# Kernel optimization log

Hardware: AMD Instinct MI355X
Metric: run time of the kernel (lower is better)

## Reference

```python
import jax, jax.numpy as jnp
import numpy as np

EPS_MSG = 1e-7   # GENConv message eps
EPS_LN = 1e-5    # LayerNorm eps

N, F_IN, D, D_OUT = 32768, 64, 512, 128


def setup_inputs() -> dict:
    key = jax.random.key(0)
    ks = jax.random.split(key, 20)
    s = 0.02
    inp = {
        "batch": jax.random.normal(ks[0], (1, N, F_IN), jnp.float32),
        "W_enc": jax.random.normal(ks[1], (F_IN, D), jnp.float32) * s,
        "b_enc": jnp.zeros((D,), jnp.float32),
        "Wf": jax.random.normal(ks[2], (D, D_OUT), jnp.float32) * s,
        "bf": jnp.zeros((D_OUT,), jnp.float32),
    }
    for l in range(2):
        inp[f"t{l}"] = jnp.array(1.0, jnp.float32)           # learnable softmax temperature
        inp[f"W1_{l}"] = jax.random.normal(ks[3 + 6 * l], (D, 2 * D), jnp.float32) * s
        inp[f"b1_{l}"] = jnp.zeros((2 * D,), jnp.float32)
        inp[f"g_{l}"] = jnp.ones((2 * D,), jnp.float32)      # LN gamma
        inp[f"be_{l}"] = jnp.zeros((2 * D,), jnp.float32)    # LN beta
        inp[f"W2_{l}"] = jax.random.normal(ks[4 + 6 * l], (2 * D, D), jnp.float32) * s
        inp[f"b2_{l}"] = jnp.zeros((D,), jnp.float32)
    return inp


def _layer_norm(z, g, b):
    mu = jnp.mean(z, axis=-1, keepdims=True)
    var = jnp.var(z, axis=-1, keepdims=True)
    return (z - mu) * jax.lax.rsqrt(var + EPS_LN) * g + b


def _deepgcn_layer(x, t, W1, b1, g, be, W2, b2):
    # res+ block: h = conv(act(norm(x))); return x + h   (norm is Identity here)
    h = jax.nn.relu(x)                       # [n, d]
    # GENConv with complete graph: msg_j = relu(h_j) + eps (independent of target i)
    m = jax.nn.relu(h) + EPS_MSG             # [n, d]
    alpha = jax.nn.softmax(t * m, axis=0)    # per-channel softmax over all source nodes
    agg = jnp.sum(alpha * m, axis=0)         # [d]  -- identical for every target node
    out = h + agg[None, :]                   # + x_dst residual inside GENConv
    # GENConv MLP: Linear(d,2d) -> LayerNorm -> ReLU -> Linear(2d,d)
    z = jax.nn.relu(_layer_norm(out @ W1 + b1, g, be))
    out = z @ W2 + b2
    return x + out


def reference(batch, W_enc, b_enc, Wf, bf,
              t0, W1_0, b1_0, g_0, be_0, W2_0, b2_0,
              t1, W1_1, b1_1, g_1, be_1, W2_1, b2_1):
    bsz, n, _ = batch.shape
    x = batch.reshape(bsz * n, -1) @ W_enc + b_enc   # node encoder
    x = _deepgcn_layer(x, t0, W1_0, b1_0, g_0, be_0, W2_0, b2_0)
    x = _deepgcn_layer(x, t1, W1_1, b1_1, g_1, be_1, W2_1, b2_1)
    x = jax.nn.relu(x)                               # layers[0].act(layers[0].norm(x)), norm=Identity
    out = x @ Wf + bf
    return out.reshape(bsz, n, -1)
```

## Files before the change

kernel.cpp:

```cpp
#include <hip/hip_runtime.h>

#define DEV __device__ __forceinline__

typedef __attribute__((ext_vector_type(8))) short s8v;
typedef __attribute__((ext_vector_type(4))) float f4v;

DEV short f2bf(float f) {
  unsigned u = __builtin_bit_cast(unsigned, f);
  u += 0x7fffu + ((u >> 16) & 1u);
  return (short)(u >> 16);
}
DEV float bf2f(short s) {
  unsigned u = ((unsigned)(unsigned short)s) << 16;
  return __builtin_bit_cast(float, u);
}

DEV f4v mfma_16x16x32_bf16(s8v a, s8v b, f4v c) {
  asm("v_mfma_f32_16x16x32_bf16 %0, %1, %2, %0" : "+v"(c) : "v"(a), "v"(b));
  return c;
}

DEV s8v relu8(s8v a) {
#pragma unroll
  for (int i = 0; i < 8; ++i) a[i] = a[i] > (short)0 ? a[i] : (short)0;
  return a;
}

__global__ __launch_bounds__(256) void tconv_k(const float* __restrict__ in,
                                               short* __restrict__ out,
                                               int K, int N) {
  __shared__ float t[64][65];
  const int nb = blockIdx.x * 64, kb = blockIdx.y * 64;
  const int c = threadIdx.x & 63, r0 = threadIdx.x >> 6;
#pragma unroll
  for (int rr = 0; rr < 64; rr += 4)
    t[rr + r0][c] = in[(size_t)(kb + rr + r0) * N + nb + c];
  __syncthreads();
#pragma unroll
  for (int rr = 0; rr < 64; rr += 4)
    out[(size_t)(nb + rr + r0) * K + kb + c] = f2bf(t[c][rr + r0]);
}

__global__ __launch_bounds__(256) void conv_k(const float* __restrict__ in,
                                              short* __restrict__ out, int n4) {
  int i = blockIdx.x * 256 + threadIdx.x;
  if (i >= n4) return;
  float4 v = ((const float4*)in)[i];
  short4 o;
  o.x = f2bf(v.x);
  o.y = f2bf(v.y);
  o.z = f2bf(v.z);
  o.w = f2bf(v.w);
  ((short4*)out)[i] = o;
}

__global__ __launch_bounds__(256) void zero_k(float* p, int n) {
  int i = blockIdx.x * 256 + threadIdx.x;
  if (i < n) p[i] = 0.f;
}

__global__ __launch_bounds__(256) void finalize_k(const float* __restrict__ sums,
                                                  const float* __restrict__ W1,
                                                  const float* __restrict__ b1,
                                                  float* __restrict__ biasEff) {
  __shared__ float agg[512];
  __shared__ float part[16][16];
  const int tid = threadIdx.x;
  for (int d = tid; d < 512; d += 256) agg[d] = sums[512 + d] / sums[d];
  __syncthreads();
  const int j = blockIdx.x * 16 + (tid & 15);
  const int grp = tid >> 4;
  float p = 0.f;
#pragma unroll 4
  for (int dd = 0; dd < 32; ++dd) {
    int d = grp * 32 + dd;
    p += agg[d] * W1[(size_t)d * 1024 + j];
  }
  part[grp][tid & 15] = p;
  __syncthreads();
  if (tid < 16) {
    float a = b1[blockIdx.x * 16 + tid];
#pragma unroll
    for (int g = 0; g < 16; ++g) a += part[g][tid];
    biasEff[blockIdx.x * 16 + tid] = a;
  }
}

__global__ __launch_bounds__(256) void ln_relu_k(short* __restrict__ z,
                                                 const float* __restrict__ g,
                                                 const float* __restrict__ be) {
  const int row = blockIdx.x * 4 + (threadIdx.x >> 6);
  const int lane = threadIdx.x & 63;
  short* zr = z + (size_t)row * 1024;
  s8v c0 = *(const s8v*)&zr[lane * 8];
  s8v c1 = *(const s8v*)&zr[512 + lane * 8];
  float v[16];
  float s = 0.f, q = 0.f;
#pragma unroll
  for (int i = 0; i < 8; ++i) { v[i] = bf2f(c0[i]); v[8 + i] = bf2f(c1[i]); }
#pragma unroll
  for (int i = 0; i < 16; ++i) { s += v[i]; q += v[i] * v[i]; }
#pragma unroll
  for (int o = 32; o > 0; o >>= 1) { s += __shfl_xor(s, o); q += __shfl_xor(q, o); }
  float mu = s * (1.f / 1024.f);
  float var = q * (1.f / 1024.f) - mu * mu;
  float rs = rsqrtf(var + 1e-5f);
  float gv[16], bv[16];
#pragma unroll
  for (int i = 0; i < 8; ++i) {
    gv[i] = g[lane * 8 + i];      gv[8 + i] = g[512 + lane * 8 + i];
    bv[i] = be[lane * 8 + i];     bv[8 + i] = be[512 + lane * 8 + i];
  }
  s8v o0, o1;
#pragma unroll
  for (int i = 0; i < 8; ++i) {
    o0[i] = f2bf(fmaxf((v[i] - mu) * rs * gv[i] + bv[i], 0.f));
    o1[i] = f2bf(fmaxf((v[8 + i] - mu) * rs * gv[8 + i] + bv[8 + i], 0.f));
  }
  *(s8v*)&zr[lane * 8] = o0;
  *(s8v*)&zr[512 + lane * 8] = o1;
}

#define F_ADD   1
#define F_WF32  2
#define F_WBF   4
#define F_SM    8
#define F_RELUA 16

template <int FLAGS>
__global__ __launch_bounds__(256) void gemm_k(const short* __restrict__ A,
                                              const short* __restrict__ Bt,
                                              const float* __restrict__ bias,
                                              const short* __restrict__ Xin,
                                              short* __restrict__ Cb,
                                              float* __restrict__ Cf,
                                              const float* __restrict__ tptr,
                                              float* __restrict__ sums,
                                              int M, int N, int K) {
  __shared__ short lA[128 * 64];
  __shared__ short lB[128 * 64];
  const int tid = threadIdx.x;
  const int lane = tid & 63, wid = tid >> 6;
  const int wr = wid >> 1, wc = wid & 1;
  const int nwg = gridDim.x * gridDim.y;
  const int wg = blockIdx.y * gridDim.x + blockIdx.x;
  const int swz = (wg & 7) * (nwg >> 3) + (wg >> 3);
  const int bx = swz % gridDim.x, by = swz / gridDim.x;
  const int brow = by * 128, bcol = bx * 128;
  const int l15 = lane & 15, lhi = lane >> 4;
  f4v acc[4][4] = {};

  for (int k0 = 0; k0 < K; k0 += 64) {
#pragma unroll
    for (int r = 0; r < 4; ++r) {
      int chunk = r * 256 + tid;
      int row = chunk >> 3;
      int kc = ((chunk & 7) ^ (row & 7)) << 3;
      const short* ga = A + (size_t)(brow + row) * K + (k0 + kc);
      const short* gb = Bt + (size_t)(bcol + row) * K + (k0 + kc);
      __builtin_amdgcn_global_load_lds(
          (const __attribute__((address_space(1))) void*)ga,
          (__attribute__((address_space(3))) void*)&lA[(r * 256 + wid * 64) * 8],
          16, 0, 0);
      __builtin_amdgcn_global_load_lds(
          (const __attribute__((address_space(1))) void*)gb,
          (__attribute__((address_space(3))) void*)&lB[(r * 256 + wid * 64) * 8],
          16, 0, 0);
    }
    __syncthreads();
#pragma unroll
    for (int kk = 0; kk < 2; ++kk) {
      s8v af[4], bfr[4];
#pragma unroll
      for (int i = 0; i < 4; ++i) {
        const int rowA = wr * 64 + i * 16 + l15;
        const int rowB = wc * 64 + i * 16 + l15;
        const int cA = ((kk * 4 + lhi) ^ (rowA & 7)) << 3;
        const int cB = ((kk * 4 + lhi) ^ (rowB & 7)) << 3;
        af[i]  = *(const s8v*)&lA[rowA * 64 + cA];
        bfr[i] = *(const s8v*)&lB[rowB * 64 + cB];
        if (FLAGS & F_RELUA) af[i] = relu8(af[i]);
      }
#pragma unroll
      for (int mi = 0; mi < 4; ++mi)
#pragma unroll
        for (int ni = 0; ni < 4; ++ni)
          acc[mi][ni] = mfma_16x16x32_bf16(af[mi], bfr[ni], acc[mi][ni]);
    }
    __syncthreads();
  }

  const float tv = (FLAGS & F_SM) ? tptr[0] : 0.f;
  float* sred = (float*)lA;
  if (FLAGS & F_SM) {
    sred[tid] = 0.f;
    __syncthreads();
  }
#pragma unroll
  for (int ni = 0; ni < 4; ++ni) {
    int col = bcol + wc * 64 + ni * 16 + l15;
    float bv = bias[col];
    float se = 0.f, sem = 0.f;
#pragma unroll
    for (int mi = 0; mi < 4; ++mi) {
#pragma unroll
      for (int r = 0; r < 4; ++r) {
        int row = brow + wr * 64 + mi * 16 + lhi * 4 + r;
        size_t idx = (size_t)row * N + col;
        float v = acc[mi][ni][r] + bv;
        if (FLAGS & F_ADD) v += bf2f(Xin[idx]);
        if (FLAGS & F_WF32) Cf[idx] = v;
        if (FLAGS & F_WBF) Cb[idx] = f2bf(v);
        if (FLAGS & F_SM) {
          float m = fmaxf(v, 0.f) + 1e-7f;
          float e = __expf(tv * m);
          se += e;
          sem += e * m;
        }
      }
    }
    if (FLAGS & F_SM) {
      se += __shfl_xor(se, 16);   se += __shfl_xor(se, 32);
      sem += __shfl_xor(sem, 16); sem += __shfl_xor(sem, 32);
      if (lhi == 0) {
        atomicAdd(&sred[wc * 64 + ni * 16 + l15], se);
        atomicAdd(&sred[128 + wc * 64 + ni * 16 + l15], sem);
      }
    }
  }
  if (FLAGS & F_SM) {
    __syncthreads();
    int v = tid >> 7, c = tid & 127;
    atomicAdd(&sums[v * 512 + bcol + c], sred[v * 128 + c]);
  }
}

extern "C" void kernel_launch(void* const* d_in, const int* in_sizes, int n_in,
                              void* d_out, int out_size, void* d_ws,
                              size_t ws_size, hipStream_t stream) {
  (void)in_sizes; (void)n_in; (void)out_size; (void)ws_size;
  const float* batch = (const float*)d_in[0];
  const float* W_enc = (const float*)d_in[1];
  const float* b_enc = (const float*)d_in[2];
  const float* Wf    = (const float*)d_in[3];
  const float* bfv   = (const float*)d_in[4];
  const float* tptr[2] = {(const float*)d_in[5],  (const float*)d_in[12]};
  const float* W1[2]   = {(const float*)d_in[6],  (const float*)d_in[13]};
  const float* b1[2]   = {(const float*)d_in[7],  (const float*)d_in[14]};
  const float* g[2]    = {(const float*)d_in[8],  (const float*)d_in[15]};
  const float* be[2]   = {(const float*)d_in[9],  (const float*)d_in[16]};
  const float* W2[2]   = {(const float*)d_in[10], (const float*)d_in[17]};
  const float* b2[2]   = {(const float*)d_in[11], (const float*)d_in[18]};
  float* out = (float*)d_out;

  const int M = 32768;
  char* ws = (char*)d_ws;
  size_t off = 0;
  auto alloc = [&](size_t bytes) -> char* {
    char* p = ws + off;
    off += (bytes + 255) & ~(size_t)255;
    return p;
  };
  short* xbf    = (short*)alloc((size_t)M * 512 * 2);
  short* zbuf   = (short*)alloc((size_t)M * 1024 * 2);
  short* bbuf   = (short*)alloc((size_t)M * 64 * 2);
  short* wencT  = (short*)alloc(512 * 64 * 2);
  short* w1T0   = (short*)alloc(1024 * 512 * 2);
  short* w2T0   = (short*)alloc(512 * 1024 * 2);
  short* w1T1   = (short*)alloc(1024 * 512 * 2);
  short* w2T1   = (short*)alloc(512 * 1024 * 2);
  short* wfT    = (short*)alloc(128 * 512 * 2);
  float* sums   = (float*)alloc(2 * 1024 * 4);
  float* biasEff= (float*)alloc(1024 * 4);
  short* w1T[2] = {w1T0, w1T1};
  short* w2T[2] = {w2T0, w2T1};

  tconv_k<<<dim3(512 / 64, 64 / 64), 256, 0, stream>>>(W_enc, wencT, 64, 512);
  tconv_k<<<dim3(1024 / 64, 512 / 64), 256, 0, stream>>>(W1[0], w1T[0], 512, 1024);
  tconv_k<<<dim3(512 / 64, 1024 / 64), 256, 0, stream>>>(W2[0], w2T[0], 1024, 512);
  tconv_k<<<dim3(1024 / 64, 512 / 64), 256, 0, stream>>>(W1[1], w1T[1], 512, 1024);
  tconv_k<<<dim3(512 / 64, 1024 / 64), 256, 0, stream>>>(W2[1], w2T[1], 1024, 512);
  tconv_k<<<dim3(128 / 64, 512 / 64), 256, 0, stream>>>(Wf, wfT, 512, 128);

  conv_k<<<(M * 64 / 4 + 255) / 256, 256, 0, stream>>>(batch, bbuf, M * 64 / 4);
  zero_k<<<(2048 + 255) / 256, 256, 0, stream>>>(sums, 2048);

  gemm_k<F_WBF | F_SM><<<dim3(512 / 128, M / 128), 256, 0, stream>>>(
      bbuf, wencT, b_enc, nullptr, xbf, nullptr, tptr[0], sums, M, 512, 64);

  for (int l = 0; l < 2; ++l) {
    finalize_k<<<64, 256, 0, stream>>>(sums + l * 1024, W1[l], b1[l], biasEff);
    gemm_k<F_WBF | F_RELUA><<<dim3(1024 / 128, M / 128), 256, 0, stream>>>(
        xbf, w1T[l], biasEff, nullptr, zbuf, nullptr, nullptr, nullptr,
        M, 1024, 512);
    ln_relu_k<<<M / 4, 256, 0, stream>>>(zbuf, g[l], be[l]);
    if (l == 0) {
      gemm_k<F_ADD | F_WBF | F_SM><<<dim3(512 / 128, M / 128), 256, 0, stream>>>(
          zbuf, w2T[l], b2[l], xbf, xbf, nullptr, tptr[1], sums + 1024,
          M, 512, 1024);
    } else {
      gemm_k<F_ADD | F_WBF><<<dim3(512 / 128, M / 128), 256, 0, stream>>>(
          zbuf, w2T[l], b2[l], xbf, xbf, nullptr, nullptr, nullptr,
          M, 512, 1024);
    }
  }

  gemm_k<F_WF32 | F_RELUA><<<dim3(128 / 128, M / 128), 256, 0, stream>>>(
      xbf, wfT, bfv, nullptr, nullptr, out, nullptr, nullptr, M, 128, 512);
}
```

Baseline: 371.6 us.

## Double-buffer LDS tiles in GEMM with explicit vmcnt waits and barriers

Splits the GEMM main loop into stage/compute phases over two LDS buffer pairs. The next K-tile's global-to-LDS loads are issued while the current tile is consumed, with explicit s_waitcnt vmcnt and s_barrier instead of __syncthreads. It also raises wave priority during the MFMA phase. This aims to hide global load latency behind matrix math, at the cost of doubling LDS use to 64KB per block, which may reduce occupancy.

```diff
diff --git a/kernel.cpp b/kernel.cpp
--- a/kernel.cpp
+++ b/kernel.cpp
@@ -127,6 +127,11 @@
 #define F_SM    8
 #define F_RELUA 16
 
+#define VM8  asm volatile("s_waitcnt vmcnt(8)" ::: "memory")
+#define VM0  asm volatile("s_waitcnt vmcnt(0)" ::: "memory")
+#define SBAR __builtin_amdgcn_s_barrier()
+#define SCH0 __builtin_amdgcn_sched_barrier(0)
+
 template <int FLAGS>
 __global__ __launch_bounds__(256) void gemm_k(const short* __restrict__ A,
                                               const short* __restrict__ Bt,
@@ -137,8 +142,10 @@
                                               const float* __restrict__ tptr,
                                               float* __restrict__ sums,
                                               int M, int N, int K) {
-  __shared__ short lA[128 * 64];
-  __shared__ short lB[128 * 64];
+  __shared__ short lA0[128 * 64];
+  __shared__ short lB0[128 * 64];
+  __shared__ short lA1[128 * 64];
+  __shared__ short lB1[128 * 64];
   const int tid = threadIdx.x;
   const int lane = tid & 63, wid = tid >> 6;
   const int wr = wid >> 1, wc = wid & 1;
@@ -150,7 +157,8 @@
   const int l15 = lane & 15, lhi = lane >> 4;
   f4v acc[4][4] = {};
 
-  for (int k0 = 0; k0 < K; k0 += 64) {
+  auto stage = [&](short* dA, short* dB, int t) {
+    const int k0 = t << 6;
 #pragma unroll
     for (int r = 0; r < 4; ++r) {
       int chunk = r * 256 + tid;
@@ -160,14 +168,17 @@
       const short* gb = Bt + (size_t)(bcol + row) * K + (k0 + kc);
       __builtin_amdgcn_global_load_lds(
           (const __attribute__((address_space(1))) void*)ga,
-          (__attribute__((address_space(3))) void*)&lA[(r * 256 + wid * 64) * 8],
+          (__attribute__((address_space(3))) void*)&dA[(r * 256 + wid * 64) * 8],
           16, 0, 0);
       __builtin_amdgcn_global_load_lds(
           (const __attribute__((address_space(1))) void*)gb,
-          (__attribute__((address_space(3))) void*)&lB[(r * 256 + wid * 64) * 8],
+          (__attribute__((address_space(3))) void*)&dB[(r * 256 + wid * 64) * 8],
           16, 0, 0);
     }
-    __syncthreads();
+  };
+
+  auto compute = [&](const short* lA, const short* lB) {
+    __builtin_amdgcn_s_setprio(1);
 #pragma unroll
     for (int kk = 0; kk < 2; ++kk) {
       s8v af[4], bfr[4];
@@ -187,11 +198,29 @@
         for (int ni = 0; ni < 4; ++ni)
           acc[mi][ni] = mfma_16x16x32_bf16(af[mi], bfr[ni], acc[mi][ni]);
     }
-    __syncthreads();
+    __builtin_amdgcn_s_setprio(0);
+  };
+
+  const int nt = K >> 6;
+  stage(lA0, lB0, 0);
+  if (nt > 1) { stage(lA1, lB1, 1); VM8; } else { VM0; }
+  SCH0; SBAR;
+
+  for (int t = 0; t < nt; t += 2) {
+    compute(lA0, lB0);
+    SBAR;
+    if (t + 2 < nt) { stage(lA0, lB0, t + 2); VM8; } else { VM0; }
+    SCH0; SBAR;
+    if (t + 1 < nt) {
+      compute(lA1, lB1);
+      SBAR;
+      if (t + 3 < nt) { stage(lA1, lB1, t + 3); VM8; } else { VM0; }
+      SCH0; SBAR;
+    }
   }
 
   const float tv = (FLAGS & F_SM) ? tptr[0] : 0.f;
-  float* sred = (float*)lA;
+  float* sred = (float*)lA0;
   if (FLAGS & F_SM) {
     sred[tid] = 0.f;
     __syncthreads();
```

New measurement: 376.9 us. Within noise of the previous version (+1.4%).

## Fuse first MLP GEMM with LayerNorm and ReLU epilogue

Applied to the files above, without the earlier changes.

Replaces the W1 GEMM plus separate LayerNorm/ReLU kernel with a single kernel where each 1024-thread block computes full 1024-wide rows for 64 nodes, then reduces row statistics across waves in shared memory and applies LN, gamma/beta and ReLU before writing bf16. This removes one full read-modify-write pass over the large intermediate z buffer and a kernel launch per layer. In exchange, the new GEMM uses a small K-step with no double buffering, reloads the whole weight slab per block, and launches fewer, larger blocks, which may lower MFMA efficiency.

```diff
diff --git a/kernel.cpp b/kernel.cpp
--- a/kernel.cpp
+++ b/kernel.cpp
@@ -25,6 +25,12 @@
   for (int i = 0; i < 8; ++i) a[i] = a[i] > (short)0 ? a[i] : (short)0;
   return a;
 }
+
+#define F_ADD   1
+#define F_WF32  2
+#define F_WBF   4
+#define F_SM    8
+#define F_RELUA 16
 
 __global__ __launch_bounds__(256) void tconv_k(const float* __restrict__ in,
                                                short* __restrict__ out,
@@ -85,47 +91,6 @@
     biasEff[blockIdx.x * 16 + tid] = a;
   }
 }
-
-__global__ __launch_bounds__(256) void ln_relu_k(short* __restrict__ z,
-                                                 const float* __restrict__ g,
-                                                 const float* __restrict__ be) {
-  const int row = blockIdx.x * 4 + (threadIdx.x >> 6);
-  const int lane = threadIdx.x & 63;
-  short* zr = z + (size_t)row * 1024;
-  s8v c0 = *(const s8v*)&zr[lane * 8];
-  s8v c1 = *(const s8v*)&zr[512 + lane * 8];
-  float v[16];
-  float s = 0.f, q = 0.f;
-#pragma unroll
-  for (int i = 0; i < 8; ++i) { v[i] = bf2f(c0[i]); v[8 + i] = bf2f(c1[i]); }
-#pragma unroll
-  for (int i = 0; i < 16; ++i) { s += v[i]; q += v[i] * v[i]; }
-#pragma unroll
-  for (int o = 32; o > 0; o >>= 1) { s += __shfl_xor(s, o); q += __shfl_xor(q, o); }
-  float mu = s * (1.f / 1024.f);
-  float var = q * (1.f / 1024.f) - mu * mu;
-  float rs = rsqrtf(var + 1e-5f);
-  float gv[16], bv[16];
-#pragma unroll
-  for (int i = 0; i < 8; ++i) {
-    gv[i] = g[lane * 8 + i];      gv[8 + i] = g[512 + lane * 8 + i];
-    bv[i] = be[lane * 8 + i];     bv[8 + i] = be[512 + lane * 8 + i];
-  }
-  s8v o0, o1;
-#pragma unroll
-  for (int i = 0; i < 8; ++i) {
-    o0[i] = f2bf(fmaxf((v[i] - mu) * rs * gv[i] + bv[i], 0.f));
-    o1[i] = f2bf(fmaxf((v[8 + i] - mu) * rs * gv[8 + i] + bv[8 + i], 0.f));
-  }
-  *(s8v*)&zr[lane * 8] = o0;
-  *(s8v*)&zr[512 + lane * 8] = o1;
-}
-
-#define F_ADD   1
-#define F_WF32  2
-#define F_WBF   4
-#define F_SM    8
-#define F_RELUA 16
 
 template <int FLAGS>
 __global__ __launch_bounds__(256) void gemm_k(const short* __restrict__ A,
@@ -235,6 +200,130 @@
   }
 }
 
+template <int FLAGS>
+__global__ __launch_bounds__(1024) void gemmln_k(const short* __restrict__ A,
+                                                 const short* __restrict__ Bt,
+                                                 const float* __restrict__ biasEff,
+                                                 const float* __restrict__ g,
+                                                 const float* __restrict__ be,
+                                                 short* __restrict__ Z,
+                                                 int M) {
+  const int K = 512, N = 1024;
+  __shared__ short lA[64 * 32];
+  __shared__ short lB[1024 * 32];
+  __shared__ float sred[2][64][8];
+  const int tid = threadIdx.x;
+  const int lane = tid & 63, wid = tid >> 6;
+  const int wr = wid >> 3, wc = wid & 7;
+  const int nwg = gridDim.x;
+  const int wg = blockIdx.x;
+  const int swz = (wg & 7) * (nwg >> 3) + (wg >> 3);
+  const int brow = swz * 64;
+  const int l15 = lane & 15, lhi = lane >> 4;
+  f4v acc[2][8] = {};
+
+  for (int k0 = 0; k0 < K; k0 += 32) {
+#pragma unroll
+    for (int r = 0; r < 4; ++r) {
+      int chunk = r * 1024 + tid;
+      int row = chunk >> 2;
+      int sw = (row & 3) ^ ((row >> 2) & 3);
+      int kc = ((chunk & 3) ^ sw) << 3;
+      __builtin_amdgcn_global_load_lds(
+          (const __attribute__((address_space(1))) void*)(Bt + (size_t)row * K + k0 + kc),
+          (__attribute__((address_space(3))) void*)&lB[(r * 1024 + wid * 64) * 8],
+          16, 0, 0);
+    }
+    if (wid < 4) {
+      int chunk = tid;
+      int row = chunk >> 2;
+      int sw = (row & 3) ^ ((row >> 2) & 3);
+      int kc = ((chunk & 3) ^ sw) << 3;
+      __builtin_amdgcn_global_load_lds(
+          (const __attribute__((address_space(1))) void*)(A + (size_t)(brow + row) * K + k0 + kc),
+          (__attribute__((address_space(3))) void*)&lA[(wid * 64) * 8],
+          16, 0, 0);
+    }
+    __syncthreads();
+    s8v af[2], bfr[8];
+#pragma unroll
+    for (int i = 0; i < 2; ++i) {
+      const int rowA = wr * 32 + i * 16 + l15;
+      const int sw = (rowA & 3) ^ ((rowA >> 2) & 3);
+      af[i] = *(const s8v*)&lA[rowA * 32 + ((lhi ^ sw) << 3)];
+      if (FLAGS & F_RELUA) af[i] = relu8(af[i]);
+    }
+#pragma unroll
+    for (int j = 0; j < 8; ++j) {
+      const int rowB = wc * 128 + j * 16 + l15;
+      const int sw = (rowB & 3) ^ ((rowB >> 2) & 3);
+      bfr[j] = *(const s8v*)&lB[rowB * 32 + ((lhi ^ sw) << 3)];
+    }
+#pragma unroll
+    for (int mi = 0; mi < 2; ++mi)
+#pragma unroll
+      for (int ni = 0; ni < 8; ++ni)
+        acc[mi][ni] = mfma_16x16x32_bf16(af[mi], bfr[ni], acc[mi][ni]);
+    __syncthreads();
+  }
+
+  float bv[8];
+#pragma unroll
+  for (int ni = 0; ni < 8; ++ni) bv[ni] = biasEff[wc * 128 + ni * 16 + l15];
+
+#pragma unroll
+  for (int mi = 0; mi < 2; ++mi) {
+#pragma unroll
+    for (int r = 0; r < 4; ++r) {
+      float s = 0.f, q = 0.f;
+#pragma unroll
+      for (int ni = 0; ni < 8; ++ni) {
+        float v = acc[mi][ni][r] + bv[ni];
+        s += v;
+        q += v * v;
+      }
+#pragma unroll
+      for (int o = 1; o < 16; o <<= 1) {
+        s += __shfl_xor(s, o);
+        q += __shfl_xor(q, o);
+      }
+      if (l15 == 0) {
+        int rowl = wr * 32 + mi * 16 + lhi * 4 + r;
+        sred[0][rowl][wc] = s;
+        sred[1][rowl][wc] = q;
+      }
+    }
+  }
+  __syncthreads();
+
+  float gv[8], bev[8];
+#pragma unroll
+  for (int ni = 0; ni < 8; ++ni) {
+    gv[ni]  = g[wc * 128 + ni * 16 + l15];
+    bev[ni] = be[wc * 128 + ni * 16 + l15];
+  }
+#pragma unroll
+  for (int mi = 0; mi < 2; ++mi) {
+#pragma unroll
+    for (int r = 0; r < 4; ++r) {
+      int rowl = wr * 32 + mi * 16 + lhi * 4 + r;
+      float S = 0.f, Q = 0.f;
+#pragma unroll
+      for (int w = 0; w < 8; ++w) { S += sred[0][rowl][w]; Q += sred[1][rowl][w]; }
+      float mu = S * (1.f / 1024.f);
+      float var = Q * (1.f / 1024.f) - mu * mu;
+      float rs = rsqrtf(var + 1e-5f);
+      short* zr = Z + (size_t)(brow + rowl) * N;
+#pragma unroll
+      for (int ni = 0; ni < 8; ++ni) {
+        float v = acc[mi][ni][r] + bv[ni];
+        float z = fmaxf((v - mu) * rs * gv[ni] + bev[ni], 0.f);
+        zr[wc * 128 + ni * 16 + l15] = f2bf(z);
+      }
+    }
+  }
+}
+
 extern "C" void kernel_launch(void* const* d_in, const int* in_sizes, int n_in,
                               void* d_out, int out_size, void* d_ws,
                               size_t ws_size, hipStream_t stream) {
@@ -290,10 +379,8 @@
 
   for (int l = 0; l < 2; ++l) {
     finalize_k<<<64, 256, 0, stream>>>(sums + l * 1024, W1[l], b1[l], biasEff);
-    gemm_k<F_WBF | F_RELUA><<<dim3(1024 / 128, M / 128), 256, 0, stream>>>(
-        xbf, w1T[l], biasEff, nullptr, zbuf, nullptr, nullptr, nullptr,
-        M, 1024, 512);
-    ln_relu_k<<<M / 4, 256, 0, stream>>>(zbuf, g[l], be[l]);
+    gemmln_k<F_RELUA><<<M / 64, 1024, 0, stream>>>(
+        xbf, w1T[l], biasEff, g[l], be[l], zbuf, M);
     if (l == 0) {
       gemm_k<F_ADD | F_WBF | F_SM><<<dim3(512 / 128, M / 128), 256, 0, stream>>>(
           zbuf, w2T[l], b2[l], xbf, xbf, nullptr, tptr[1], sums + 1024,
```

Result: slower. 439.6 us (+18.3%).
